# Performance work log

Hardware: AMD Instinct MI355X
Metric: run time of the kernel (lower is better)

Reference implementation:

```python
import jax, jax.numpy as jnp
import numpy as np

DICT_SIZE = 512
EMBED_DIM = 64
SPARSITY = 5
COMMITMENT_COST = 0.25
EPSILON = 1e-10
COEFF_CLAMP = 1e7


def setup_inputs() -> dict:
    key = jax.random.key(0)
    kz, kd = jax.random.split(key)
    z = jax.random.normal(kz, (32, EMBED_DIM, 32, 32), dtype=jnp.float32)
    D = jax.random.normal(kd, (EMBED_DIM, DICT_SIZE), dtype=jnp.float32)
    # _normalize_dictionary(): unit L2 norm per atom (column)
    D = D / jnp.linalg.norm(D, axis=0, keepdims=True)
    return {"z": z, "dictionary": D}


def batch_omp(signals, dictionary):
    # signals: [E, N], dictionary: [E, K]
    E, N = signals.shape
    K = dictionary.shape[1]
    Dt = dictionary.T  # [K, E]
    DtD = Dt @ dictionary + EPSILON * jnp.eye(K, dtype=signals.dtype)  # [K, K]
    residual = signals
    active = jnp.zeros((N, K), dtype=bool)
    coefficients = jnp.zeros((N, K), dtype=signals.dtype)
    idx = jnp.zeros((N, 0), dtype=jnp.int32)
    rows = jnp.arange(N)
    for k in range(SPARSITY):  # small fixed unroll; active-set size is static k+1
        corr = Dt @ residual                                  # [K, N]
        corr = jnp.where(active.T, -jnp.inf, corr)
        new_atoms = jnp.argmax(corr, axis=0).astype(jnp.int32)  # [N]
        active = active.at[rows, new_atoms].set(True)
        idx = jnp.concatenate([idx, new_atoms[:, None]], axis=1)  # [N, k+1]
        G = DtD[idx[:, :, None], idx[:, None, :]]             # [N, k+1, k+1]
        y = jnp.einsum('nke,en->nk', Dt[idx], residual)       # [N, k+1]
        coeffs = jnp.linalg.solve(G, y[..., None])[..., 0]    # [N, k+1]
        update = jnp.einsum('enk,nk->en', dictionary[:, idx], coeffs)  # [E, N]
        residual = signals - update
        coefficients = coefficients.at[rows[:, None], idx].set(coeffs)
    return coefficients.T  # [K, N]


def reference(z, dictionary):
    B, E, H, W = z.shape
    # [B,E,H,W] -> [E, N]
    z_flat = z.transpose(0, 2, 3, 1).reshape(-1, E).T
    # sparse coding is done under no_grad in torch
    coefficients = jax.lax.stop_gradient(batch_omp(z_flat, dictionary))
    coefficients = jnp.clip(coefficients, -COEFF_CLAMP, COEFF_CLAMP)  # [K, N]
    z_q_flat = dictionary @ coefficients                               # [E, N]
    z_q_reshaped = z_q_flat.T.reshape(B, H, W, E).transpose(0, 3, 1, 2)
    rec_loss = jnp.mean((jax.lax.stop_gradient(z_q_flat) - z_flat) ** 2)
    commit_loss = jnp.mean((z_q_flat - jax.lax.stop_gradient(z_flat)) ** 2)
    effective_cost = COMMITMENT_COST * (1.0 + SPARSITY / 10.0)
    coeff_loss = jnp.mean(jnp.abs(coefficients))
    loss = rec_loss + effective_cost * commit_loss + 0.001 * coeff_loss
    # straight-through estimator with clamp
    z_q = z + jax.lax.stop_gradient(jnp.clip(z_q_reshaped - z, -1.0, 1.0))
    return z_q, loss, coefficients
```

## Files before the change

kernel.cpp:

```cpp
#include <hip/hip_runtime.h>
#include <math.h>

#define NSIG 32768
#define KD   512
#define ED   64
#define SP   5

__global__ __launch_bounds__(256) void k_pre(const float* __restrict__ D,
                                             double* __restrict__ DtD,
                                             float* __restrict__ DtDf,
                                             float4* __restrict__ coef4) {
  if (blockIdx.x < 1024) {
    int flat = blockIdx.x * 256 + threadIdx.x;
    int i = flat >> 9, j = flat & 511;
    double acc = 0.0;
    #pragma unroll
    for (int e = 0; e < ED; ++e)
      acc += (double)D[e * KD + i] * (double)D[e * KD + j];
    if (i == j) acc += 1e-10;
    DtD[flat] = acc;
    DtDf[flat] = (float)acc;
  } else {
    size_t count4 = (size_t)KD * NSIG / 4;
    size_t i = (size_t)(blockIdx.x - 1024) * 256 + threadIdx.x;
    size_t stride = (size_t)2048 * 256;
    float4 zv = make_float4(0.f, 0.f, 0.f, 0.f);
    for (; i < count4; i += stride) coef4[i] = zv;
  }
}

template <int K>
__device__ __forceinline__ void omp_iter64(const double* __restrict__ DtD,
                                           const double (&c0)[16], unsigned& amask,
                                           int (&idx)[SP], double (&cc)[SP],
                                           double (&tri)[15], double (&c0sel)[SP],
                                           int li) {
  double vb = -INFINITY;
  int ab = 0x7FFFFFFF;
  #pragma unroll
  for (int j4 = 0; j4 < 4; ++j4) {
    int a0 = (j4 << 7) + (li << 2);
    double v0 = c0[4 * j4], v1 = c0[4 * j4 + 1];
    double v2 = c0[4 * j4 + 2], v3 = c0[4 * j4 + 3];
    #pragma unroll
    for (int m = 0; m < K; ++m) {
      const double* gp = DtD + (size_t)idx[m] * KD + a0;
      double2 gA = *(const double2*)gp;
      double2 gB = *(const double2*)(gp + 2);
      v0 -= gA.x * cc[m];
      v1 -= gA.y * cc[m];
      v2 -= gB.x * cc[m];
      v3 -= gB.y * cc[m];
    }
    v0 = ((amask >> (4 * j4 + 0)) & 1u) ? -INFINITY : v0;
    v1 = ((amask >> (4 * j4 + 1)) & 1u) ? -INFINITY : v1;
    v2 = ((amask >> (4 * j4 + 2)) & 1u) ? -INFINITY : v2;
    v3 = ((amask >> (4 * j4 + 3)) & 1u) ? -INFINITY : v3;
    if (v0 > vb) { vb = v0; ab = a0; }
    if (v1 > vb) { vb = v1; ab = a0 + 1; }
    if (v2 > vb) { vb = v2; ab = a0 + 2; }
    if (v3 > vb) { vb = v3; ab = a0 + 3; }
  }
  #pragma unroll
  for (int s = 16; s >= 1; s >>= 1) {
    double ov = __shfl_xor(vb, s, 64);
    int    oa = __shfl_xor(ab, s, 64);
    if (ov > vb || (ov == vb && oa < ab)) { vb = ov; ab = oa; }
  }
  idx[K] = ab;
  if (((ab >> 2) & 31) == li) amask |= 1u << ((((ab >> 7) << 2)) | (ab & 3));
  const double* drow = DtD + (size_t)ab * KD;
  double bb[SP], u[SP];
  #pragma unroll
  for (int m = 0; m < K; ++m) bb[m] = drow[idx[m]];
  {
    double csel = vb;
    #pragma unroll
    for (int m = 0; m < K; ++m) csel += bb[m] * cc[m];
    c0sel[K] = csel;
  }
  double sch = drow[ab];
  #pragma unroll
  for (int i = 0; i < K; ++i) {
    double ui = 0.0;
    #pragma unroll
    for (int m = 0; m < K; ++m) {
      int lo = i < m ? i : m, hi = i < m ? m : i;
      ui += tri[lo * SP - lo * (lo + 1) / 2 + hi] * bb[m];
    }
    u[i] = ui;
    sch -= bb[i] * ui;
  }
  double r = 1.0 / sch;
  #pragma unroll
  for (int i = 0; i < K; ++i) {
    #pragma unroll
    for (int j = i; j < K; ++j) tri[i * SP - i * (i + 1) / 2 + j] += r * u[i] * u[j];
    tri[i * SP - i * (i + 1) / 2 + K] = -r * u[i];
  }
  tri[K * SP - K * (K + 1) / 2 + K] = r;
  double h[SP];
  #pragma unroll
  for (int i = 0; i <= K; ++i) {
    double s = 0.0;
    #pragma unroll
    for (int j = 0; j <= K; ++j) {
      int lo = i < j ? i : j, hi = i < j ? j : i;
      s += tri[lo * SP - lo * (lo + 1) / 2 + hi] * c0sel[j];
    }
    h[i] = s;
  }
  #pragma unroll
  for (int i = 0; i < K; ++i) cc[i] = h[i] - cc[i];
  cc[K] = h[K];
}

template <int K>
__device__ __forceinline__ void omp_iter32(const double* __restrict__ DtD,
                                           const float* __restrict__ DtDf,
                                           const float* __restrict__ Dg,
                                           const float* __restrict__ zbuf,
                                           int myS,
                                           const float (&c0f)[16], unsigned& amask,
                                           int (&idx)[SP], double (&cc)[SP],
                                           double (&tri)[15], double (&c0sel)[SP],
                                           int li, int& redoFlag) {
  float ccf[SP];
  #pragma unroll
  for (int m = 0; m < K; ++m) ccf[m] = (float)cc[m];
  float v1 = -INFINITY, v2 = -INFINITY;
  int a1 = 0x7FFFFFFF;
  #pragma unroll
  for (int j4 = 0; j4 < 4; ++j4) {
    int a0 = (j4 << 7) + (li << 2);
    float gv[SP][4];
    #pragma unroll
    for (int m = 0; m < K; ++m) {
      float4 q = *(const float4*)(DtDf + (size_t)idx[m] * KD + a0);
      gv[m][0] = q.x; gv[m][1] = q.y; gv[m][2] = q.z; gv[m][3] = q.w;
    }
    #pragma unroll
    for (int bit = 0; bit < 4; ++bit) {
      float v = c0f[4 * j4 + bit];
      #pragma unroll
      for (int m = 0; m < K; ++m) v -= gv[m][bit] * ccf[m];
      v = ((amask >> (4 * j4 + bit)) & 1u) ? -INFINITY : v;
      if (v > v1) { v2 = v1; v1 = v; a1 = a0 + bit; }
      else v2 = fmaxf(v2, v);
    }
  }
  #pragma unroll
  for (int s = 16; s >= 1; s >>= 1) {
    float ov1 = __shfl_xor(v1, s, 64);
    int   oa1 = __shfl_xor(a1, s, 64);
    float ov2 = __shfl_xor(v2, s, 64);
    bool oWins = (ov1 > v1) || (ov1 == v1 && oa1 < a1);
    float loserTop = oWins ? v1 : ov1;
    if (oWins) { v1 = ov1; a1 = oa1; }
    v2 = fmaxf(fmaxf(v2, ov2), loserTop);
  }
  float ccmax = 0.0f;
  #pragma unroll
  for (int m = 0; m < K; ++m) ccmax = fmaxf(ccmax, fabsf(ccf[m]));
  float tau = 2e-4f + 2e-5f * ccmax;
  if (!(v1 - v2 >= tau)) redoFlag = 1;
  int ab = a1;
  idx[K] = ab;
  if (((ab >> 2) & 31) == li) amask |= 1u << ((((ab >> 7) << 2)) | (ab & 3));
  {
    int e0 = li << 1;
    double part = (double)Dg[e0 * KD + ab] * (double)zbuf[e0 * 16 + myS]
                + (double)Dg[(e0 + 1) * KD + ab] * (double)zbuf[(e0 + 1) * 16 + myS];
    #pragma unroll
    for (int s = 16; s >= 1; s >>= 1) part += __shfl_xor(part, s, 64);
    c0sel[K] = part;
  }
  const double* drow = DtD + (size_t)ab * KD;
  double bb[SP], u[SP];
  #pragma unroll
  for (int m = 0; m < K; ++m) bb[m] = drow[idx[m]];
  double sch = drow[ab];
  #pragma unroll
  for (int i = 0; i < K; ++i) {
    double ui = 0.0;
    #pragma unroll
    for (int m = 0; m < K; ++m) {
      int lo = i < m ? i : m, hi = i < m ? m : i;
      ui += tri[lo * SP - lo * (lo + 1) / 2 + hi] * bb[m];
    }
    u[i] = ui;
    sch -= bb[i] * ui;
  }
  double r = 1.0 / sch;
  #pragma unroll
  for (int i = 0; i < K; ++i) {
    #pragma unroll
    for (int j = i; j < K; ++j) tri[i * SP - i * (i + 1) / 2 + j] += r * u[i] * u[j];
    tri[i * SP - i * (i + 1) / 2 + K] = -r * u[i];
  }
  tri[K * SP - K * (K + 1) / 2 + K] = r;
  double h[SP];
  #pragma unroll
  for (int i = 0; i <= K; ++i) {
    double s = 0.0;
    #pragma unroll
    for (int j = 0; j <= K; ++j) {
      int lo = i < j ? i : j, hi = i < j ? j : i;
      s += tri[lo * SP - lo * (lo + 1) / 2 + hi] * c0sel[j];
    }
    h[i] = s;
  }
  #pragma unroll
  for (int i = 0; i < K; ++i) cc[i] = h[i] - cc[i];
  cc[K] = h[K];
}

__global__ __launch_bounds__(512) void k_fused(const float* __restrict__ z,
                                               const float* __restrict__ D,
                                               const double* __restrict__ DtD,
                                               const float* __restrict__ DtDf,
                                               float* __restrict__ coefOut,
                                               int* __restrict__ idxWs,
                                               double* __restrict__ cWs,
                                               double* __restrict__ csumWs,
                                               int* __restrict__ flagWs) {
  __shared__ float zbuf[64 * 16];
  int tid = threadIdx.x;
  int lane = tid & 63;
  int wv = tid >> 6;
  int li = lane & 31;
  int g  = lane >> 5;
  int myS = 2 * wv + g;
  int n = blockIdx.x * 16 + myS;
  {
    int n0 = blockIdx.x * 16;
    int b = n0 >> 10, p0 = n0 & 1023;
    const float* zb = z + (size_t)b * 65536 + p0;
    #pragma unroll
    for (int k2 = 0; k2 < 2; ++k2) {
      int f = tid + 512 * k2;
      zbuf[f] = zb[(f >> 4) * 1024 + (f & 15)];
    }
  }
  __syncthreads();
  float cA[8], cB[8];
  #pragma unroll
  for (int p = 0; p < 8; ++p) { cA[p] = 0.0f; cB[p] = 0.0f; }
  const float* Dbase = D + lane * 4;
  #pragma unroll 8
  for (int e = 0; e < ED; ++e) {
    float2 zz = *(const float2*)(zbuf + e * 16 + 2 * wv);
    float zA = zz.x, zB = zz.y;
    float4 d0 = *(const float4*)(Dbase + e * 512);
    float4 d1 = *(const float4*)(Dbase + e * 512 + 256);
    float dv[8] = {d0.x, d0.y, d0.z, d0.w, d1.x, d1.y, d1.z, d1.w};
    #pragma unroll
    for (int p = 0; p < 8; ++p) {
      cA[p] += zA * dv[p];
      cB[p] += zB * dv[p];
    }
  }
  float c0f[16];
  #pragma unroll
  for (int j4 = 0; j4 < 4; ++j4) {
    int src = ((j4 & 1) << 5) + li;
    #pragma unroll
    for (int bit = 0; bit < 4; ++bit) {
      float tA = __shfl(cA[((j4 >> 1) << 2) + bit], src, 64);
      float tB = __shfl(cB[((j4 >> 1) << 2) + bit], src, 64);
      c0f[4 * j4 + bit] = g ? tB : tA;
    }
  }
  unsigned amask = 0;
  int redoFlag = 0;
  int idx[SP]; double cc[SP]; double tri[15]; double c0sel[SP];
  omp_iter32<0>(DtD, DtDf, D, zbuf, myS, c0f, amask, idx, cc, tri, c0sel, li, redoFlag);
  omp_iter32<1>(DtD, DtDf, D, zbuf, myS, c0f, amask, idx, cc, tri, c0sel, li, redoFlag);
  omp_iter32<2>(DtD, DtDf, D, zbuf, myS, c0f, amask, idx, cc, tri, c0sel, li, redoFlag);
  omp_iter32<3>(DtD, DtDf, D, zbuf, myS, c0f, amask, idx, cc, tri, c0sel, li, redoFlag);
  omp_iter32<4>(DtD, DtDf, D, zbuf, myS, c0f, amask, idx, cc, tri, c0sel, li, redoFlag);
  if (li == 0) {
    double cs = 0.0;
    #pragma unroll
    for (int j = 0; j < SP; ++j) {
      double cj = cc[j];
      cj = fmin(fmax(cj, -10000000.0), 10000000.0);
      cs += fabs(cj);
      idxWs[n * SP + j] = idx[j];
      cWs[n * SP + j] = cj;
      coefOut[(size_t)idx[j] * NSIG + n] = (float)cj;
    }
    csumWs[n] = cs;
    flagWs[n] = redoFlag;
  }
}

__global__ __launch_bounds__(512) void k_redo(const float* __restrict__ z,
                                              const float* __restrict__ D,
                                              const double* __restrict__ DtD,
                                              const int* __restrict__ flagWs,
                                              float* __restrict__ coefOut,
                                              int* __restrict__ idxWs,
                                              double* __restrict__ cWs,
                                              double* __restrict__ csumWs) {
  int tid = threadIdx.x;
  int lane = tid & 63;
  int wv = tid >> 6;
  int li = lane & 31;
  int g  = lane >> 5;
  int n = blockIdx.x * 16 + 2 * wv + g;
  if (!flagWs[n]) return;
  int b = n >> 10, p = n & 1023;
  const float* zp = z + (size_t)b * 65536 + p;
  double c0[16];
  #pragma unroll
  for (int j = 0; j < 16; ++j) c0[j] = 0.0;
  for (int e = 0; e < ED; ++e) {
    double zv = (double)zp[e * 1024];
    #pragma unroll
    for (int j4 = 0; j4 < 4; ++j4) {
      float4 dv = *(const float4*)(D + e * KD + (j4 << 7) + (li << 2));
      c0[4 * j4 + 0] += zv * (double)dv.x;
      c0[4 * j4 + 1] += zv * (double)dv.y;
      c0[4 * j4 + 2] += zv * (double)dv.z;
      c0[4 * j4 + 3] += zv * (double)dv.w;
    }
  }
  unsigned amask = 0;
  int idx[SP]; double cc[SP]; double tri[15]; double c0sel[SP];
  omp_iter64<0>(DtD, c0, amask, idx, cc, tri, c0sel, li);
  omp_iter64<1>(DtD, c0, amask, idx, cc, tri, c0sel, li);
  omp_iter64<2>(DtD, c0, amask, idx, cc, tri, c0sel, li);
  omp_iter64<3>(DtD, c0, amask, idx, cc, tri, c0sel, li);
  omp_iter64<4>(DtD, c0, amask, idx, cc, tri, c0sel, li);
  if (li == 0) {
    #pragma unroll
    for (int j = 0; j < SP; ++j)
      coefOut[(size_t)idxWs[n * SP + j] * NSIG + n] = 0.0f;
    double cs = 0.0;
    #pragma unroll
    for (int j = 0; j < SP; ++j) {
      double cj = cc[j];
      cj = fmin(fmax(cj, -10000000.0), 10000000.0);
      cs += fabs(cj);
      idxWs[n * SP + j] = idx[j];
      cWs[n * SP + j] = cj;
      coefOut[(size_t)idx[j] * NSIG + n] = (float)cj;
    }
    csumWs[n] = cs;
  }
}

__global__ __launch_bounds__(256) void k_zq(const float* __restrict__ z,
                                            const float* __restrict__ D,
                                            const int* __restrict__ idxWs,
                                            const double* __restrict__ cWs,
                                            float* __restrict__ zqOut,
                                            double* __restrict__ recWs) {
  int t = threadIdx.x;
  size_t flat = (size_t)blockIdx.x * 256 + t;
  int b = (int)(flat >> 16);
  int e = (int)((flat >> 10) & 63);
  int p = (int)(flat & 1023);
  int n = b * 1024 + p;
  double u = 0.0;
  #pragma unroll
  for (int j = 0; j < SP; ++j) {
    int a = idxWs[n * SP + j];
    u += (double)D[e * KD + a] * cWs[n * SP + j];
  }
  float zv = z[flat];
  double d = u - (double)zv;
  double dc = fmin(fmax(d, -1.0), 1.0);
  zqOut[flat] = (float)((double)zv + dc);
  __shared__ double red[256];
  red[t] = d * d;
  __syncthreads();
  #pragma unroll
  for (int s = 128; s >= 1; s >>= 1) {
    if (t < s) red[t] += red[t + s];
    __syncthreads();
  }
  if (t == 0) recWs[blockIdx.x] = red[0];
}

__global__ __launch_bounds__(256) void k_loss(const double* __restrict__ recWs,
                                              const double* __restrict__ csumWs,
                                              float* __restrict__ lossOut) {
  int t = threadIdx.x;
  double r = 0.0, c = 0.0;
  for (int i = t; i < 8192; i += 256) r += recWs[i];
  for (int i = t; i < NSIG; i += 256) c += csumWs[i];
  __shared__ double red[512];
  red[t] = r; red[256 + t] = c;
  __syncthreads();
  #pragma unroll
  for (int s = 128; s >= 1; s >>= 1) {
    if (t < s) { red[t] += red[t + s]; red[256 + t] += red[256 + t + s]; }
    __syncthreads();
  }
  if (t == 0) {
    double rec = red[0] / (double)(64.0 * 32768.0);
    double cm  = red[256] / (double)(512.0 * 32768.0);
    double loss = rec + 0.375 * rec + 0.001 * cm;
    lossOut[0] = (float)loss;
  }
}

extern "C" void kernel_launch(void* const* d_in, const int* in_sizes, int n_in,
                              void* d_out, int out_size, void* d_ws, size_t ws_size,
                              hipStream_t stream) {
  const float* z = (const float*)d_in[0];
  const float* D = (const float*)d_in[1];
  float* out = (float*)d_out;
  float* zqOut   = out;
  float* lossOut = out + 2097152;
  float* coefOut = out + 2097153;

  char* w = (char*)d_ws;
  double* DtD    = (double*)w; w += (size_t)KD * KD * 8;
  float*  DtDf   = (float*)w;  w += (size_t)KD * KD * 4;
  int*    idxWs  = (int*)w;    w += (size_t)NSIG * SP * 4;
  double* cWs    = (double*)w; w += (size_t)NSIG * SP * 8;
  double* csumWs = (double*)w; w += (size_t)NSIG * 8;
  double* recWs  = (double*)w; w += (size_t)8192 * 8;
  int*    flagWs = (int*)w;    w += (size_t)NSIG * 4;

  k_pre<<<3072, 256, 0, stream>>>(D, DtD, DtDf, (float4*)coefOut);
  k_fused<<<NSIG / 16, 512, 0, stream>>>(z, D, DtD, DtDf, coefOut, idxWs, cWs,
                                         csumWs, flagWs);
  k_redo<<<NSIG / 16, 512, 0, stream>>>(z, D, DtD, flagWs, coefOut, idxWs, cWs,
                                        csumWs);
  k_zq<<<8192, 256, 0, stream>>>(z, D, idxWs, cWs, zqOut, recWs);
  k_loss<<<1, 256, 0, stream>>>(recWs, csumWs, lossOut);
}
```

Measured before the change: 252.5 us.

## Fuse coef zeroing into OMP kernel, fold loss into zq, derive selected correlation algebraically

The coefficient-buffer zeroing moves from the precompute kernel into the fused OMP kernel, so each block clears its own 16 columns. The final loss reduction is folded into the z_q kernel using an atomic last-block counter, which removes one kernel launch. The selected atom's initial correlation is now rebuilt from the winning residual correlation plus the DtD row times the current coefficients, instead of a global D-times-z dot product with shuffle reductions. The redo tolerance is also widened, which may send more signals down the slower redo path.

Measured after the change: 435.1 us. +72.3%, slower.

```diff
diff --git a/kernel.cpp b/kernel.cpp
--- a/kernel.cpp
+++ b/kernel.cpp
@@ -6,27 +6,20 @@
 #define ED   64
 #define SP   5
 
-__global__ __launch_bounds__(256) void k_pre(const float* __restrict__ D,
+__global__ __launch_bounds__(256) void k_dtd(const float* __restrict__ D,
                                              double* __restrict__ DtD,
                                              float* __restrict__ DtDf,
-                                             float4* __restrict__ coef4) {
-  if (blockIdx.x < 1024) {
-    int flat = blockIdx.x * 256 + threadIdx.x;
-    int i = flat >> 9, j = flat & 511;
-    double acc = 0.0;
-    #pragma unroll
-    for (int e = 0; e < ED; ++e)
-      acc += (double)D[e * KD + i] * (double)D[e * KD + j];
-    if (i == j) acc += 1e-10;
-    DtD[flat] = acc;
-    DtDf[flat] = (float)acc;
-  } else {
-    size_t count4 = (size_t)KD * NSIG / 4;
-    size_t i = (size_t)(blockIdx.x - 1024) * 256 + threadIdx.x;
-    size_t stride = (size_t)2048 * 256;
-    float4 zv = make_float4(0.f, 0.f, 0.f, 0.f);
-    for (; i < count4; i += stride) coef4[i] = zv;
-  }
+                                             int* __restrict__ counter) {
+  if (blockIdx.x == 0 && threadIdx.x == 0) *counter = 0;
+  int flat = blockIdx.x * 256 + threadIdx.x;
+  int i = flat >> 9, j = flat & 511;
+  double acc = 0.0;
+  #pragma unroll
+  for (int e = 0; e < ED; ++e)
+    acc += (double)D[e * KD + i] * (double)D[e * KD + j];
+  if (i == j) acc += 1e-10;
+  DtD[flat] = acc;
+  DtDf[flat] = (float)acc;
 }
 
 template <int K>
@@ -118,9 +111,6 @@
 template <int K>
 __device__ __forceinline__ void omp_iter32(const double* __restrict__ DtD,
                                            const float* __restrict__ DtDf,
-                                           const float* __restrict__ Dg,
-                                           const float* __restrict__ zbuf,
-                                           int myS,
                                            const float (&c0f)[16], unsigned& amask,
                                            int (&idx)[SP], double (&cc)[SP],
                                            double (&tri)[15], double (&c0sel)[SP],
@@ -162,23 +152,21 @@
   float ccmax = 0.0f;
   #pragma unroll
   for (int m = 0; m < K; ++m) ccmax = fmaxf(ccmax, fabsf(ccf[m]));
-  float tau = 2e-4f + 2e-5f * ccmax;
+  float tau = 2e-4f + 1e-4f * ccmax;
   if (!(v1 - v2 >= tau)) redoFlag = 1;
   int ab = a1;
   idx[K] = ab;
   if (((ab >> 2) & 31) == li) amask |= 1u << ((((ab >> 7) << 2)) | (ab & 3));
-  {
-    int e0 = li << 1;
-    double part = (double)Dg[e0 * KD + ab] * (double)zbuf[e0 * 16 + myS]
-                + (double)Dg[(e0 + 1) * KD + ab] * (double)zbuf[(e0 + 1) * 16 + myS];
-    #pragma unroll
-    for (int s = 16; s >= 1; s >>= 1) part += __shfl_xor(part, s, 64);
-    c0sel[K] = part;
-  }
   const double* drow = DtD + (size_t)ab * KD;
   double bb[SP], u[SP];
   #pragma unroll
   for (int m = 0; m < K; ++m) bb[m] = drow[idx[m]];
+  {
+    double csel = (double)v1;
+    #pragma unroll
+    for (int m = 0; m < K; ++m) csel += bb[m] * cc[m];
+    c0sel[K] = csel;
+  }
   double sch = drow[ab];
   #pragma unroll
   for (int i = 0; i < K; ++i) {
@@ -231,9 +219,18 @@
   int li = lane & 31;
   int g  = lane >> 5;
   int myS = 2 * wv + g;
-  int n = blockIdx.x * 16 + myS;
+  int n0 = blockIdx.x * 16;
+  int n = n0 + myS;
   {
-    int n0 = blockIdx.x * 16;
+    float4 zv4 = make_float4(0.f, 0.f, 0.f, 0.f);
+    #pragma unroll
+    for (int i = 0; i < 4; ++i) {
+      int f4 = tid + 512 * i;
+      int a = f4 >> 2, s4 = f4 & 3;
+      *(float4*)(coefOut + (size_t)a * NSIG + n0 + s4 * 4) = zv4;
+    }
+  }
+  {
     int b = n0 >> 10, p0 = n0 & 1023;
     const float* zb = z + (size_t)b * 65536 + p0;
     #pragma unroll
@@ -274,11 +271,11 @@
   unsigned amask = 0;
   int redoFlag = 0;
   int idx[SP]; double cc[SP]; double tri[15]; double c0sel[SP];
-  omp_iter32<0>(DtD, DtDf, D, zbuf, myS, c0f, amask, idx, cc, tri, c0sel, li, redoFlag);
-  omp_iter32<1>(DtD, DtDf, D, zbuf, myS, c0f, amask, idx, cc, tri, c0sel, li, redoFlag);
-  omp_iter32<2>(DtD, DtDf, D, zbuf, myS, c0f, amask, idx, cc, tri, c0sel, li, redoFlag);
-  omp_iter32<3>(DtD, DtDf, D, zbuf, myS, c0f, amask, idx, cc, tri, c0sel, li, redoFlag);
-  omp_iter32<4>(DtD, DtDf, D, zbuf, myS, c0f, amask, idx, cc, tri, c0sel, li, redoFlag);
+  omp_iter32<0>(DtD, DtDf, c0f, amask, idx, cc, tri, c0sel, li, redoFlag);
+  omp_iter32<1>(DtD, DtDf, c0f, amask, idx, cc, tri, c0sel, li, redoFlag);
+  omp_iter32<2>(DtD, DtDf, c0f, amask, idx, cc, tri, c0sel, li, redoFlag);
+  omp_iter32<3>(DtD, DtDf, c0f, amask, idx, cc, tri, c0sel, li, redoFlag);
+  omp_iter32<4>(DtD, DtDf, c0f, amask, idx, cc, tri, c0sel, li, redoFlag);
   if (li == 0) {
     double cs = 0.0;
     #pragma unroll
@@ -355,8 +352,11 @@
                                             const float* __restrict__ D,
                                             const int* __restrict__ idxWs,
                                             const double* __restrict__ cWs,
+                                            const double* __restrict__ csumWs,
                                             float* __restrict__ zqOut,
-                                            double* __restrict__ recWs) {
+                                            double* __restrict__ recWs,
+                                            float* __restrict__ lossOut,
+                                            int* __restrict__ counter) {
   int t = threadIdx.x;
   size_t flat = (size_t)blockIdx.x * 256 + t;
   int b = (int)(flat >> 16);
@@ -373,7 +373,7 @@
   double d = u - (double)zv;
   double dc = fmin(fmax(d, -1.0), 1.0);
   zqOut[flat] = (float)((double)zv + dc);
-  __shared__ double red[256];
+  __shared__ double red[512];
   red[t] = d * d;
   __syncthreads();
   #pragma unroll
@@ -381,17 +381,18 @@
     if (t < s) red[t] += red[t + s];
     __syncthreads();
   }
-  if (t == 0) recWs[blockIdx.x] = red[0];
-}
-
-__global__ __launch_bounds__(256) void k_loss(const double* __restrict__ recWs,
-                                              const double* __restrict__ csumWs,
-                                              float* __restrict__ lossOut) {
-  int t = threadIdx.x;
+  __shared__ int isLast;
+  if (t == 0) {
+    recWs[blockIdx.x] = red[0];
+    __threadfence();
+    isLast = (atomicAdd(counter, 1) == 8191);
+  }
+  __syncthreads();
+  if (!isLast) return;
+  __threadfence();
   double r = 0.0, c = 0.0;
   for (int i = t; i < 8192; i += 256) r += recWs[i];
   for (int i = t; i < NSIG; i += 256) c += csumWs[i];
-  __shared__ double red[512];
   red[t] = r; red[256 + t] = c;
   __syncthreads();
   #pragma unroll
@@ -425,12 +426,13 @@
   double* csumWs = (double*)w; w += (size_t)NSIG * 8;
   double* recWs  = (double*)w; w += (size_t)8192 * 8;
   int*    flagWs = (int*)w;    w += (size_t)NSIG * 4;
-
-  k_pre<<<3072, 256, 0, stream>>>(D, DtD, DtDf, (float4*)coefOut);
+  int*    counter = (int*)w;   w += 64;
+
+  k_dtd<<<1024, 256, 0, stream>>>(D, DtD, DtDf, counter);
   k_fused<<<NSIG / 16, 512, 0, stream>>>(z, D, DtD, DtDf, coefOut, idxWs, cWs,
                                          csumWs, flagWs);
   k_redo<<<NSIG / 16, 512, 0, stream>>>(z, D, DtD, flagWs, coefOut, idxWs, cWs,
                                         csumWs);
-  k_zq<<<8192, 256, 0, stream>>>(z, D, idxWs, cWs, zqOut, recWs);
-  k_loss<<<1, 256, 0, stream>>>(recWs, csumWs, lossOut);
-}
+  k_zq<<<8192, 256, 0, stream>>>(z, D, idxWs, cWs, csumWs, zqOut, recWs,
+                                 lossOut, counter);
+}
```
